# Optimization experiments

Hardware: AMD Instinct MI355X
Metric: run time of the kernel (lower is better)

Reference implementation:

```python
import jax, jax.numpy as jnp
from jax import lax
import numpy as np

B, S, D, H = 512, 512, 64, 32


def _lstm_layer(x, W_ih, W_hh, b_ih, b_hh):
    """PyTorch-convention LSTM layer. x: [B,S,Din] -> hs: [B,S,H].
    Gate order i,f,g,o; W_ih: [4H,Din], W_hh: [4H,H], biases [4H]."""
    Bn = x.shape[0]
    Hn = W_hh.shape[1]
    # Precompute all input projections in one big GEMM: [B,S,4H]
    gx = jnp.einsum('bsd,gd->bsg', x, W_ih) + b_ih + b_hh
    gx = jnp.swapaxes(gx, 0, 1)  # [S,B,4H] for scan over time

    def step(carry, g_t):
        h, c = carry
        g = g_t + h @ W_hh.T  # [B,4H]
        i, f, gg, o = jnp.split(g, 4, axis=-1)
        i = jax.nn.sigmoid(i)
        f = jax.nn.sigmoid(f)
        gg = jnp.tanh(gg)
        o = jax.nn.sigmoid(o)
        c = f * c + i * gg
        h = o * jnp.tanh(c)
        return (h, c), h

    h0 = jnp.zeros((Bn, Hn), x.dtype)
    c0 = jnp.zeros((Bn, Hn), x.dtype)
    _, hs = lax.scan(step, (h0, c0), gx)
    return jnp.swapaxes(hs, 0, 1)  # [B,S,H]


def setup_inputs() -> dict:
    key = jax.random.key(0)
    ks = jax.random.split(key, 12)
    s_in = 1.0 / np.sqrt(H)  # PyTorch LSTM init scale
    inp = {
        'x': jax.random.normal(ks[0], (B, S, D), jnp.float32),
        'W_ih0': jax.random.uniform(ks[1], (4 * H, D), jnp.float32, -s_in, s_in),
        'W_hh0': jax.random.uniform(ks[2], (4 * H, H), jnp.float32, -s_in, s_in),
        'b_ih0': jax.random.uniform(ks[3], (4 * H,), jnp.float32, -s_in, s_in),
        'b_hh0': jax.random.uniform(ks[4], (4 * H,), jnp.float32, -s_in, s_in),
        'W_ih1': jax.random.uniform(ks[5], (4 * H, H), jnp.float32, -s_in, s_in),
        'W_hh1': jax.random.uniform(ks[6], (4 * H, H), jnp.float32, -s_in, s_in),
        'b_ih1': jax.random.uniform(ks[7], (4 * H,), jnp.float32, -s_in, s_in),
        'b_hh1': jax.random.uniform(ks[8], (4 * H,), jnp.float32, -s_in, s_in),
        'W_fc': jax.random.uniform(ks[9], (1, H), jnp.float32, -s_in, s_in),
        'b_fc': jax.random.uniform(ks[10], (1,), jnp.float32, -s_in, s_in),
    }
    return inp


def reference(x, W_ih0, W_hh0, b_ih0, b_hh0, W_ih1, W_hh1, b_ih1, b_hh1, W_fc, b_fc):
    h1 = _lstm_layer(x, W_ih0, W_hh0, b_ih0, b_hh0)   # [B,S,H]
    h2 = _lstm_layer(h1, W_ih1, W_hh1, b_ih1, b_hh1)  # [B,S,H]
    last = h2[:, -1, :]  # dropout is identity in eval mode
    return last @ W_fc.T + b_fc  # [B,1]
```

## Files before the change

### kernel.cpp

```cpp
#include <hip/hip_runtime.h>
#include <hip/hip_fp16.h>

#define B_SZ  512
#define S_LEN 512
#define D_IN  64
#define H_DIM 32
#define KPIPE 8
#define NSUPER (S_LEN / KPIPE)

typedef _Float16 h2 __attribute__((ext_vector_type(2)));

__device__ __forceinline__ float fsig(float x) {
    float e = __builtin_amdgcn_exp2f(x * -1.44269504088896340736f);
    return __builtin_amdgcn_rcpf(1.0f + e);
}
__device__ __forceinline__ float ftanh(float x) {
    float e = __builtin_amdgcn_exp2f(x * -2.88539008177792681472f);
    return __builtin_fmaf(2.0f, __builtin_amdgcn_rcpf(1.0f + e), -1.0f);
}

#if __has_builtin(__builtin_amdgcn_fdot2)
__device__ __forceinline__ float fdot2(h2 a, h2 b, float c) {
    return __builtin_amdgcn_fdot2(a, b, c, false);
}
#else
__device__ __forceinline__ float fdot2(h2 a, h2 b, float c) {
    return __builtin_fmaf((float)a[1], (float)b[1],
           __builtin_fmaf((float)a[0], (float)b[0], c));
}
#endif

__device__ __forceinline__ h2 u2h2(unsigned int u) { return __builtin_bit_cast(h2, u); }
__device__ __forceinline__ unsigned int pk16(float x, float y) {
    unsigned int lo = __half_as_ushort(__float2half_rn(x));
    unsigned int hi = __half_as_ushort(__float2half_rn(y));
    return lo | (hi << 16);
}

__device__ __forceinline__ float dpp_swap1(float x) {
    return __builtin_bit_cast(float, __builtin_amdgcn_mov_dpp(
        __builtin_bit_cast(int, x), 0xB1, 0xF, 0xF, false));
}

#define LDS_ORDER() asm volatile("" ::: "memory")
#define LGKM_FENCE() asm volatile("s_waitcnt lgkmcnt(0)" ::: "memory")
#define VM_FENCE()   asm volatile("s_waitcnt vmcnt(0)" ::: "memory")

__global__ __launch_bounds__(192, 1) void lstm_scan_kernel(
    const float* __restrict__ x,
    const float* __restrict__ Wih0,
    const float* __restrict__ Whh0,
    const float* __restrict__ bih0,
    const float* __restrict__ bhh0,
    const float* __restrict__ Wih1,
    const float* __restrict__ Whh1,
    const float* __restrict__ bih1,
    const float* __restrict__ bhh1,
    const float* __restrict__ Wfc,
    const float* __restrict__ bfc,
    float* __restrict__ out)
{
    const int tid  = threadIdx.x;
    const int lane = tid & 63;
    const int j    = lane >> 1;
    const int p    = lane & 1;
    const int b    = blockIdx.x;
    const int rA   = p ? (32 + j) : j;
    const int rB   = rA + 64;

    __shared__ unsigned short h0buf[2][KPIPE][32];
    __shared__ unsigned short h1sm[32];
    __shared__ unsigned int   xbuf[KPIPE][32];
    __shared__ unsigned int   gxbuf[2][KPIPE][64];

    const float sclB = p ? -1.44269504088896340736f : -2.88539008177792681472f;
    const float mulB = p ?  1.0f : 2.0f;
    const float addB = p ?  0.0f : -1.0f;

    if (tid < 64) {
        unsigned int wh0A[16], wh0B[16];
        #pragma unroll
        for (int k4 = 0; k4 < 8; ++k4) {
            float4 v;
            v = reinterpret_cast<const float4*>(Whh0 + rA * 32)[k4];
            wh0A[2*k4+0] = pk16(v.x, v.y);  wh0A[2*k4+1] = pk16(v.z, v.w);
            v = reinterpret_cast<const float4*>(Whh0 + rB * 32)[k4];
            wh0B[2*k4+0] = pk16(v.x, v.y);  wh0B[2*k4+1] = pk16(v.z, v.w);
        }
        #pragma unroll
        for (int k = 0; k < 16; ++k)
            asm volatile("" : "+v"(wh0A[k]), "+v"(wh0B[k]));

        h2 h0p[16];
        #pragma unroll
        for (int k = 0; k < 16; ++k) h0p[k] = (h2){0, 0};
        float c0 = 0.f;
        float zA = 0.f, zB = 0.f;

        LGKM_FENCE();
        __builtin_amdgcn_s_barrier();

        for (int s = 0; s < NSUPER; ++s) {
            unsigned int gxr[KPIPE];
            LDS_ORDER();
            #pragma unroll
            for (int u = 0; u < KPIPE; ++u) gxr[u] = gxbuf[s & 1][u][lane];
            LDS_ORDER();

            unsigned short (*slot)[32] = h0buf[s & 1];
            #pragma unroll
            for (int u = 0; u < KPIPE; ++u) {
                h2 g = u2h2(gxr[u]);
                const float aA = zA + (float)g[0];
                const float aB = zB + (float)g[1];

                const float vA = fsig(aA);
                float vB;
                { float e = __builtin_amdgcn_exp2f(sclB * aB);
                  vB = __builtin_fmaf(mulB, __builtin_amdgcn_rcpf(1.0f + e), addB); }
                const float nA = dpp_swap1(vA);
                const float nB = dpp_swap1(vB);
                const float iv = p ? nA : vA;
                const float fv = p ? vA : nA;
                const float gv = p ? nB : vB;
                const float ov = p ? vB : nB;
                c0 = __builtin_fmaf(fv, c0, iv * gv);
                const float h0 = ov * ftanh(c0);

                LDS_ORDER();
                slot[u][j] = (unsigned short)__half_as_ushort(__float2half_rn(h0));
                LDS_ORDER();
                {
                    const uint4* hp = reinterpret_cast<const uint4*>(&slot[u][0]);
                    uint4 a0 = hp[0], a1 = hp[1], a2 = hp[2], a3 = hp[3];
                    h0p[ 0]=u2h2(a0.x); h0p[ 1]=u2h2(a0.y); h0p[ 2]=u2h2(a0.z); h0p[ 3]=u2h2(a0.w);
                    h0p[ 4]=u2h2(a1.x); h0p[ 5]=u2h2(a1.y); h0p[ 6]=u2h2(a1.z); h0p[ 7]=u2h2(a1.w);
                    h0p[ 8]=u2h2(a2.x); h0p[ 9]=u2h2(a2.y); h0p[10]=u2h2(a2.z); h0p[11]=u2h2(a2.w);
                    h0p[12]=u2h2(a3.x); h0p[13]=u2h2(a3.y); h0p[14]=u2h2(a3.z); h0p[15]=u2h2(a3.w);
                }

                float zA0 = 0.f, zA1 = 0.f, zB0 = 0.f, zB1 = 0.f;
                #pragma unroll
                for (int k = 0; k < 16; k += 2) {
                    zA0 = fdot2(h0p[k],   u2h2(wh0A[k]),   zA0);
                    zA1 = fdot2(h0p[k+1], u2h2(wh0A[k+1]), zA1);
                    zB0 = fdot2(h0p[k],   u2h2(wh0B[k]),   zB0);
                    zB1 = fdot2(h0p[k+1], u2h2(wh0B[k+1]), zB1);
                }
                zA = zA0 + zA1;  zB = zB0 + zB1;
            }
            LGKM_FENCE();
            __builtin_amdgcn_s_barrier();
        }
    } else if (tid < 128) {
        unsigned int wi1A[16], wi1B[16], wh1A[16], wh1B[16];
        #pragma unroll
        for (int k4 = 0; k4 < 8; ++k4) {
            float4 v;
            v = reinterpret_cast<const float4*>(Wih1 + rA * 32)[k4];
            wi1A[2*k4+0] = pk16(v.x, v.y);  wi1A[2*k4+1] = pk16(v.z, v.w);
            v = reinterpret_cast<const float4*>(Wih1 + rB * 32)[k4];
            wi1B[2*k4+0] = pk16(v.x, v.y);  wi1B[2*k4+1] = pk16(v.z, v.w);
            v = reinterpret_cast<const float4*>(Whh1 + rA * 32)[k4];
            wh1A[2*k4+0] = pk16(v.x, v.y);  wh1A[2*k4+1] = pk16(v.z, v.w);
            v = reinterpret_cast<const float4*>(Whh1 + rB * 32)[k4];
            wh1B[2*k4+0] = pk16(v.x, v.y);  wh1B[2*k4+1] = pk16(v.z, v.w);
        }
        #pragma unroll
        for (int k = 0; k < 16; ++k)
            asm volatile("" : "+v"(wi1A[k]), "+v"(wi1B[k]),
                              "+v"(wh1A[k]), "+v"(wh1B[k]));

        const float b1A = bih1[rA] + bhh1[rA];
        const float b1B = bih1[rB] + bhh1[rB];

        h2 h1p[16];
        #pragma unroll
        for (int k = 0; k < 16; ++k) h1p[k] = (h2){0, 0};
        float c1 = 0.f;
        float h1last = 0.f;

        auto consume8 = [&](const unsigned short (*slot)[32]) {
            uint4 d0, d1, d2, d3;
            {
                const uint4* hq = reinterpret_cast<const uint4*>(&slot[0][0]);
                d0 = hq[0]; d1 = hq[1]; d2 = hq[2]; d3 = hq[3];
            }
            #pragma unroll
            for (int u = 0; u < KPIPE; ++u) {
                h2 h0q[16];
                h0q[ 0]=u2h2(d0.x); h0q[ 1]=u2h2(d0.y); h0q[ 2]=u2h2(d0.z); h0q[ 3]=u2h2(d0.w);
                h0q[ 4]=u2h2(d1.x); h0q[ 5]=u2h2(d1.y); h0q[ 6]=u2h2(d1.z); h0q[ 7]=u2h2(d1.w);
                h0q[ 8]=u2h2(d2.x); h0q[ 9]=u2h2(d2.y); h0q[10]=u2h2(d2.z); h0q[11]=u2h2(d2.w);
                h0q[12]=u2h2(d3.x); h0q[13]=u2h2(d3.y); h0q[14]=u2h2(d3.z); h0q[15]=u2h2(d3.w);
                if (u + 1 < KPIPE) {
                    const uint4* hq = reinterpret_cast<const uint4*>(&slot[u + 1][0]);
                    d0 = hq[0]; d1 = hq[1]; d2 = hq[2]; d3 = hq[3];
                }

                float qA0 = b1A, qA1 = 0.f, qB0 = b1B, qB1 = 0.f;
                #pragma unroll
                for (int k = 0; k < 16; k += 2) {
                    qA0 = fdot2(h0q[k],   u2h2(wi1A[k]),   qA0);
                    qA1 = fdot2(h0q[k+1], u2h2(wi1A[k+1]), qA1);
                    qB0 = fdot2(h0q[k],   u2h2(wi1B[k]),   qB0);
                    qB1 = fdot2(h0q[k+1], u2h2(wi1B[k+1]), qB1);
                }
                #pragma unroll
                for (int k = 0; k < 16; k += 2) {
                    qA0 = fdot2(h1p[k],   u2h2(wh1A[k]),   qA0);
                    qA1 = fdot2(h1p[k+1], u2h2(wh1A[k+1]), qA1);
                    qB0 = fdot2(h1p[k],   u2h2(wh1B[k]),   qB0);
                    qB1 = fdot2(h1p[k+1], u2h2(wh1B[k+1]), qB1);
                }
                const float qA = qA0 + qA1;
                const float qB = qB0 + qB1;

                const float wA = fsig(qA);
                float wB;
                { float e = __builtin_amdgcn_exp2f(sclB * qB);
                  wB = __builtin_fmaf(mulB, __builtin_amdgcn_rcpf(1.0f + e), addB); }
                const float mA = dpp_swap1(wA);
                const float mB = dpp_swap1(wB);
                const float iv1 = p ? mA : wA;
                const float fv1 = p ? wA : mA;
                const float gv1 = p ? mB : wB;
                const float ov1 = p ? wB : mB;
                c1 = __builtin_fmaf(fv1, c1, iv1 * gv1);
                const float h1 = ov1 * ftanh(c1);
                h1last = h1;

                LDS_ORDER();
                h1sm[j] = (unsigned short)__half_as_ushort(__float2half_rn(h1));
                LDS_ORDER();
                {
                    const uint4* hp = reinterpret_cast<const uint4*>(h1sm);
                    uint4 a0 = hp[0], a1 = hp[1], a2 = hp[2], a3 = hp[3];
                    h1p[ 0]=u2h2(a0.x); h1p[ 1]=u2h2(a0.y); h1p[ 2]=u2h2(a0.z); h1p[ 3]=u2h2(a0.w);
                    h1p[ 4]=u2h2(a1.x); h1p[ 5]=u2h2(a1.y); h1p[ 6]=u2h2(a1.z); h1p[ 7]=u2h2(a1.w);
                    h1p[ 8]=u2h2(a2.x); h1p[ 9]=u2h2(a2.y); h1p[10]=u2h2(a2.z); h1p[11]=u2h2(a2.w);
                    h1p[12]=u2h2(a3.x); h1p[13]=u2h2(a3.y); h1p[14]=u2h2(a3.z); h1p[15]=u2h2(a3.w);
                }
            }
        };

        LGKM_FENCE();
        __builtin_amdgcn_s_barrier();
        for (int s = 0; s < NSUPER; ++s) {
            if (s > 0) consume8(h0buf[(s - 1) & 1]);
            LGKM_FENCE();
            __builtin_amdgcn_s_barrier();
        }
        consume8(h0buf[(NSUPER - 1) & 1]);

        float pFC = p ? 0.0f : h1last * Wfc[j];
        pFC += __shfl_xor(pFC, 32);
        pFC += __shfl_xor(pFC, 16);
        pFC += __shfl_xor(pFC, 8);
        pFC += __shfl_xor(pFC, 4);
        pFC += __shfl_xor(pFC, 2);
        pFC += __shfl_xor(pFC, 1);
        if (lane == 0) out[b] = pFC + bfc[0];
    } else {
        unsigned int wi0A[32], wi0B[32];
        #pragma unroll
        for (int k4 = 0; k4 < 16; ++k4) {
            float4 v;
            v = reinterpret_cast<const float4*>(Wih0 + rA * 64)[k4];
            wi0A[2*k4+0] = pk16(v.x, v.y);  wi0A[2*k4+1] = pk16(v.z, v.w);
            v = reinterpret_cast<const float4*>(Wih0 + rB * 64)[k4];
            wi0B[2*k4+0] = pk16(v.x, v.y);  wi0B[2*k4+1] = pk16(v.z, v.w);
        }
        #pragma unroll
        for (int k = 0; k < 32; ++k)
            asm volatile("" : "+v"(wi0A[k]), "+v"(wi0B[k]));

        const float b0A = bih0[rA] + bhh0[rA];
        const float b0B = bih0[rB] + bhh0[rB];

        const float* xrow = x + (size_t)b * S_LEN * 64;
        const int tsub = lane >> 3;
        const int kq   = (lane & 7) * 4;

        auto stage = [&](float4 xr0, float4 xr1) {
            uint4 w;
            w.x = pk16(xr0.x, xr0.y);  w.y = pk16(xr0.z, xr0.w);
            w.z = pk16(xr1.x, xr1.y);  w.w = pk16(xr1.z, xr1.w);
            LDS_ORDER();
            *reinterpret_cast<uint4*>(&xbuf[tsub][kq]) = w;
            LDS_ORDER();
        };
        auto compute_block = [&](unsigned int (*dst)[64]) {
            #pragma unroll
            for (int u = 0; u < KPIPE; ++u) {
                uint4 xv[8];
                #pragma unroll
                for (int q = 0; q < 8; ++q)
                    xv[q] = reinterpret_cast<const uint4*>(&xbuf[u][0])[q];
                float gA0 = b0A, gA1 = 0.f, gB0 = b0B, gB1 = 0.f;
                #pragma unroll
                for (int q = 0; q < 8; ++q) {
                    gA0 = fdot2(u2h2(xv[q].x), u2h2(wi0A[4*q+0]), gA0);
                    gA1 = fdot2(u2h2(xv[q].y), u2h2(wi0A[4*q+1]), gA1);
                    gA0 = fdot2(u2h2(xv[q].z), u2h2(wi0A[4*q+2]), gA0);
                    gA1 = fdot2(u2h2(xv[q].w), u2h2(wi0A[4*q+3]), gA1);
                    gB0 = fdot2(u2h2(xv[q].x), u2h2(wi0B[4*q+0]), gB0);
                    gB1 = fdot2(u2h2(xv[q].y), u2h2(wi0B[4*q+1]), gB1);
                    gB0 = fdot2(u2h2(xv[q].z), u2h2(wi0B[4*q+2]), gB0);
                    gB1 = fdot2(u2h2(xv[q].w), u2h2(wi0B[4*q+3]), gB1);
                }
                LDS_ORDER();
                dst[u][lane] = pk16(gA0 + gA1, gB0 + gB1);
                LDS_ORDER();
            }
        };

        float4 xr0 = reinterpret_cast<const float4*>(xrow + lane * 8)[0];
        float4 xr1 = reinterpret_cast<const float4*>(xrow + lane * 8 + 4)[0];
        VM_FENCE();
        stage(xr0, xr1);
        compute_block(gxbuf[0]);
        xr0 = reinterpret_cast<const float4*>(xrow + 512 + lane * 8)[0];
        xr1 = reinterpret_cast<const float4*>(xrow + 512 + lane * 8 + 4)[0];

        LGKM_FENCE();
        __builtin_amdgcn_s_barrier();

        for (int s = 0; s < NSUPER; ++s) {
            VM_FENCE();
            stage(xr0, xr1);
            compute_block(gxbuf[(s + 1) & 1]);
            const int sn = (s + 2 < NSUPER) ? (s + 2) : (NSUPER - 1);
            xr0 = reinterpret_cast<const float4*>(xrow + sn * 512 + lane * 8)[0];
            xr1 = reinterpret_cast<const float4*>(xrow + sn * 512 + lane * 8 + 4)[0];
            LGKM_FENCE();
            __builtin_amdgcn_s_barrier();
        }
    }
}

extern "C" void kernel_launch(void* const* d_in, const int* in_sizes, int n_in,
                              void* d_out, int out_size, void* d_ws, size_t ws_size,
                              hipStream_t stream) {
    (void)in_sizes; (void)n_in; (void)out_size; (void)d_ws; (void)ws_size;
    const float* x    = (const float*)d_in[0];
    const float* Wih0 = (const float*)d_in[1];
    const float* Whh0 = (const float*)d_in[2];
    const float* bih0 = (const float*)d_in[3];
    const float* bhh0 = (const float*)d_in[4];
    const float* Wih1 = (const float*)d_in[5];
    const float* Whh1 = (const float*)d_in[6];
    const float* bih1 = (const float*)d_in[7];
    const float* bhh1 = (const float*)d_in[8];
    const float* Wfc  = (const float*)d_in[9];
    const float* bfc  = (const float*)d_in[10];
    float* out = (float*)d_out;

    hipLaunchKernelGGL(lstm_scan_kernel, dim3(B_SZ), dim3(192), 0, stream,
                       x, Wih0, Whh0, bih0, bhh0, Wih1, Whh1, bih1, bhh1,
                       Wfc, bfc, out);
}
```

Baseline: 197.6 us.

## Double pipeline depth to 16 steps and prioritize recurrent waves

Raises the number of timesteps handled between barriers from 8 to 16, which halves the superstep barriers. The x-staging loads are reworked so each lane fetches 16 floats for the larger block. The two recurrent-layer waves get raised scheduling priority via s_setprio. The layer-1 gate dot products now use separate accumulators for the input and recurrent terms, which shortens the dependency chain. The cost is more LDS per buffer and more registers for the x loads.

Result: slower. 214.6 us (+8.6%).

```diff
diff --git a/kernel.cpp b/kernel.cpp
--- a/kernel.cpp
+++ b/kernel.cpp
@@ -5,7 +5,7 @@
 #define S_LEN 512
 #define D_IN  64
 #define H_DIM 32
-#define KPIPE 8
+#define KPIPE 16
 #define NSUPER (S_LEN / KPIPE)
 
 typedef _Float16 h2 __attribute__((ext_vector_type(2)));
@@ -78,6 +78,7 @@
     const float addB = p ?  0.0f : -1.0f;
 
     if (tid < 64) {
+        __builtin_amdgcn_s_setprio(1);
         unsigned int wh0A[16], wh0B[16];
         #pragma unroll
         for (int k4 = 0; k4 < 8; ++k4) {
@@ -153,6 +154,7 @@
             __builtin_amdgcn_s_barrier();
         }
     } else if (tid < 128) {
+        __builtin_amdgcn_s_setprio(1);
         unsigned int wi1A[16], wi1B[16], wh1A[16], wh1B[16];
         #pragma unroll
         for (int k4 = 0; k4 < 8; ++k4) {
@@ -180,7 +182,7 @@
         float c1 = 0.f;
         float h1last = 0.f;
 
-        auto consume8 = [&](const unsigned short (*slot)[32]) {
+        auto consumeK = [&](const unsigned short (*slot)[32]) {
             uint4 d0, d1, d2, d3;
             {
                 const uint4* hq = reinterpret_cast<const uint4*>(&slot[0][0]);
@@ -199,6 +201,7 @@
                 }
 
                 float qA0 = b1A, qA1 = 0.f, qB0 = b1B, qB1 = 0.f;
+                float sA0 = 0.f, sA1 = 0.f, sB0 = 0.f, sB1 = 0.f;
                 #pragma unroll
                 for (int k = 0; k < 16; k += 2) {
                     qA0 = fdot2(h0q[k],   u2h2(wi1A[k]),   qA0);
@@ -208,13 +211,13 @@
                 }
                 #pragma unroll
                 for (int k = 0; k < 16; k += 2) {
-                    qA0 = fdot2(h1p[k],   u2h2(wh1A[k]),   qA0);
-                    qA1 = fdot2(h1p[k+1], u2h2(wh1A[k+1]), qA1);
-                    qB0 = fdot2(h1p[k],   u2h2(wh1B[k]),   qB0);
-                    qB1 = fdot2(h1p[k+1], u2h2(wh1B[k+1]), qB1);
-                }
-                const float qA = qA0 + qA1;
-                const float qB = qB0 + qB1;
+                    sA0 = fdot2(h1p[k],   u2h2(wh1A[k]),   sA0);
+                    sA1 = fdot2(h1p[k+1], u2h2(wh1A[k+1]), sA1);
+                    sB0 = fdot2(h1p[k],   u2h2(wh1B[k]),   sB0);
+                    sB1 = fdot2(h1p[k+1], u2h2(wh1B[k+1]), sB1);
+                }
+                const float qA = (qA0 + qA1) + (sA0 + sA1);
+                const float qB = (qB0 + qB1) + (sB0 + sB1);
 
                 const float wA = fsig(qA);
                 float wB;
@@ -247,11 +250,11 @@
         LGKM_FENCE();
         __builtin_amdgcn_s_barrier();
         for (int s = 0; s < NSUPER; ++s) {
-            if (s > 0) consume8(h0buf[(s - 1) & 1]);
+            if (s > 0) consumeK(h0buf[(s - 1) & 1]);
             LGKM_FENCE();
             __builtin_amdgcn_s_barrier();
         }
-        consume8(h0buf[(NSUPER - 1) & 1]);
+        consumeK(h0buf[(NSUPER - 1) & 1]);
 
         float pFC = p ? 0.0f : h1last * Wfc[j];
         pFC += __shfl_xor(pFC, 32);
@@ -279,15 +282,26 @@
         const float b0B = bih0[rB] + bhh0[rB];
 
         const float* xrow = x + (size_t)b * S_LEN * 64;
-        const int tsub = lane >> 3;
-        const int kq   = (lane & 7) * 4;
-
-        auto stage = [&](float4 xr0, float4 xr1) {
-            uint4 w;
-            w.x = pk16(xr0.x, xr0.y);  w.y = pk16(xr0.z, xr0.w);
-            w.z = pk16(xr1.x, xr1.y);  w.w = pk16(xr1.z, xr1.w);
+        const int tsub = lane >> 2;
+        const int kq   = (lane & 3) * 8;
+
+        float4 xr0, xr1, xr2, xr3;
+        auto issue_loads = [&](int blk) {
+            const float* base = xrow + (size_t)blk * (KPIPE * 64) + lane * 16;
+            xr0 = reinterpret_cast<const float4*>(base)[0];
+            xr1 = reinterpret_cast<const float4*>(base + 4)[0];
+            xr2 = reinterpret_cast<const float4*>(base + 8)[0];
+            xr3 = reinterpret_cast<const float4*>(base + 12)[0];
+        };
+        auto stage = [&]() {
+            uint4 w0, w1;
+            w0.x = pk16(xr0.x, xr0.y);  w0.y = pk16(xr0.z, xr0.w);
+            w0.z = pk16(xr1.x, xr1.y);  w0.w = pk16(xr1.z, xr1.w);
+            w1.x = pk16(xr2.x, xr2.y);  w1.y = pk16(xr2.z, xr2.w);
+            w1.z = pk16(xr3.x, xr3.y);  w1.w = pk16(xr3.z, xr3.w);
             LDS_ORDER();
-            *reinterpret_cast<uint4*>(&xbuf[tsub][kq]) = w;
+            *reinterpret_cast<uint4*>(&xbuf[tsub][kq])     = w0;
+            *reinterpret_cast<uint4*>(&xbuf[tsub][kq + 4]) = w1;
             LDS_ORDER();
         };
         auto compute_block = [&](unsigned int (*dst)[64]) {
@@ -315,24 +329,20 @@
             }
         };
 
-        float4 xr0 = reinterpret_cast<const float4*>(xrow + lane * 8)[0];
-        float4 xr1 = reinterpret_cast<const float4*>(xrow + lane * 8 + 4)[0];
+        issue_loads(0);
         VM_FENCE();
-        stage(xr0, xr1);
+        stage();
         compute_block(gxbuf[0]);
-        xr0 = reinterpret_cast<const float4*>(xrow + 512 + lane * 8)[0];
-        xr1 = reinterpret_cast<const float4*>(xrow + 512 + lane * 8 + 4)[0];
+        issue_loads(1 < NSUPER ? 1 : 0);
 
         LGKM_FENCE();
         __builtin_amdgcn_s_barrier();
 
         for (int s = 0; s < NSUPER; ++s) {
             VM_FENCE();
-            stage(xr0, xr1);
+            stage();
             compute_block(gxbuf[(s + 1) & 1]);
-            const int sn = (s + 2 < NSUPER) ? (s + 2) : (NSUPER - 1);
-            xr0 = reinterpret_cast<const float4*>(xrow + sn * 512 + lane * 8)[0];
-            xr1 = reinterpret_cast<const float4*>(xrow + sn * 512 + lane * 8 + 4)[0];
+            issue_loads((s + 2 < NSUPER) ? (s + 2) : (NSUPER - 1));
             LGKM_FENCE();
             __builtin_amdgcn_s_barrier();
         }
```
